# Kernel tuning notes

Hardware: AMD Instinct MI355X
Metric: run time of the kernel (lower is better)

The kernel has to match this reference:

```python
import jax, jax.numpy as jnp
import numpy as np

C_S, C_Z, C_ATOM, H, RBF = 128, 64, 16, 4, 16
N_RES, E_RES, N_ATOM, E_ATOM = 1000, 4000, 14000, 784000


def _p(key, shape, scale=0.05):
    return (jax.random.normal(key, shape, dtype=jnp.float32) * scale)


def setup_inputs() -> dict:
    key = jax.random.key(0)
    ks = jax.random.split(key, 24)
    inp = {
        "node_features": jax.random.normal(ks[0], (N_RES, C_S), dtype=jnp.float32),
        "res_edge_features": jax.random.normal(ks[1], (E_RES, C_Z), dtype=jnp.float32),
        "res_edge_index": jax.random.randint(ks[2], (2, E_RES), 0, N_RES),
        "atom_features": jax.random.normal(ks[3], (N_ATOM, C_ATOM), dtype=jnp.float32),
        "atom_coords": jax.random.normal(ks[4], (N_ATOM, 3), dtype=jnp.float32),
        "cross_atom_edge_index": jax.random.randint(ks[5], (2, E_ATOM), 0, N_ATOM),
        "atom_edge_to_res_edge": jax.random.randint(ks[6], (E_ATOM,), 0, E_RES),
        # atom_dist_embed MLP: RBF -> RBF -> RBF -> H
        "rbf_w1": _p(ks[7], (RBF, RBF)), "rbf_b1": jnp.zeros((RBF,), jnp.float32),
        "rbf_w2": _p(ks[8], (RBF, RBF)), "rbf_b2": jnp.zeros((RBF,), jnp.float32),
        "rbf_w3": _p(ks[9], (RBF, H)),  "rbf_b3": jnp.zeros((H,), jnp.float32),
        # res_level_bias MLP: (2*c_s + c_z) -> c_atom -> H
        "rb_w1": _p(ks[10], (2 * C_S + C_Z, C_ATOM)), "rb_b1": jnp.zeros((C_ATOM,), jnp.float32),
        "rb_w2": _p(ks[11], (C_ATOM, H)), "rb_b2": jnp.zeros((H,), jnp.float32),
        # q / kv / out projections
        "wq": _p(ks[12], (C_ATOM, C_ATOM * H)),     "bq": jnp.zeros((C_ATOM * H,), jnp.float32),
        "wkv": _p(ks[13], (C_ATOM, 2 * C_ATOM * H)), "bkv": jnp.zeros((2 * C_ATOM * H,), jnp.float32),
        "wo": _p(ks[14], (C_ATOM * H, C_ATOM)),     "bo": jnp.zeros((C_ATOM,), jnp.float32),
    }
    return inp


def _rbf(d, d_min=0.0, d_max=20.0, d_count=RBF):
    mu = jnp.linspace(d_min, d_max, d_count, dtype=jnp.float32)
    sigma = (d_max - d_min) / d_count
    return jnp.exp(-(((d[..., None] - mu) / sigma) ** 2))


def _seg_softmax(x, idx, n_seg):
    # scatter-softmax over segments (pyg_utils.softmax), per head column
    m = jax.ops.segment_max(x, idx, num_segments=n_seg)
    e = jnp.exp(x - m[idx])
    s = jax.ops.segment_sum(e, idx, num_segments=n_seg)
    return e / (s[idx] + 1e-16)


def reference(node_features, res_edge_features, res_edge_index, atom_features,
              atom_coords, cross_atom_edge_index, atom_edge_to_res_edge,
              rbf_w1, rbf_b1, rbf_w2, rbf_b2, rbf_w3, rbf_b3,
              rb_w1, rb_b1, rb_w2, rb_b2, wq, bq, wkv, bkv, wo, bo,
              eps=1e-8):
    src = cross_atom_edge_index[1]
    dst = cross_atom_edge_index[0]

    # RBF distance bias  [E_atom, H]
    vec = atom_coords[dst] - atom_coords[src]
    d = jnp.linalg.norm(vec + eps, axis=-1)
    h = jax.nn.relu(_rbf(d) @ rbf_w1 + rbf_b1)
    h = jax.nn.relu(h @ rbf_w2 + rbf_b2)
    atom_dist_bias = h @ rbf_w3 + rbf_b3

    # residue-level bias  [E_res, H]
    cat = jnp.concatenate([res_edge_features,
                           node_features[res_edge_index[0]],
                           node_features[res_edge_index[1]]], axis=-1)
    res_level_bias = jax.nn.relu(cat @ rb_w1 + rb_b1) @ rb_w2 + rb_b2

    # gathered q / k / v  [E_atom, H, c_atom]
    q = (atom_features @ wq + bq)[src].reshape(-1, H, C_ATOM)
    kv = (atom_features @ wkv + bkv)[dst].reshape(-1, H, 2 * C_ATOM)
    k, v = kv[..., :C_ATOM], kv[..., C_ATOM:]

    R = jnp.einsum('ehc,ehc->eh', q, k) / np.sqrt(C_ATOM)
    R = R + res_level_bias[atom_edge_to_res_edge] + atom_dist_bias

    # atom-level scatter-softmax over edges grouped by src atom
    alpha = _seg_softmax(R, src, N_ATOM)

    # residue-level: scatter-mean of scores per residue edge, then softmax by dst res
    cnt = jax.ops.segment_sum(jnp.ones((R.shape[0],), R.dtype),
                              atom_edge_to_res_edge, num_segments=E_RES)
    block_r = jax.ops.segment_sum(R, atom_edge_to_res_edge, num_segments=E_RES)
    block_r = block_r / jnp.clip(cnt, 1.0)[:, None]
    beta = _seg_softmax(block_r, res_edge_index[1], N_RES)

    w = alpha * beta[atom_edge_to_res_edge]           # [E_atom, H]
    atom_update = jax.ops.segment_sum(w[..., None] * v, src, num_segments=N_ATOM)
    return atom_update.reshape(-1, H * C_ATOM) @ wo + bo
```

## Files before the change

### kernel.cpp

```cpp
#include <hip/hip_runtime.h>

#define NH 4
#define N_RES 1000
#define E_RES 4000
#define N_ATOM 14000
#define E_ATOM 784000
#define MAXS 128
#define NBRE 256
#define TABN 16385
#define TINV 512.0f
#define NHB 256
#define EPB 3063

#define PROJ_BLKS ((N_ATOM * 192 + 255) / 256)
#define RLB_BLKS (E_RES / 4)
#define TAB_BLKS ((TABN + 255) / 256)

typedef float f32x4 __attribute__((ext_vector_type(4)));

__device__ __forceinline__ unsigned enc_f(float f) {
  unsigned u = __float_as_uint(f);
  return (u & 0x80000000u) ? ~u : (u | 0x80000000u);
}
__device__ __forceinline__ float dec_f(unsigned e) {
  unsigned u = (e & 0x80000000u) ? (e & 0x7FFFFFFFu) : ~e;
  return __uint_as_float(u);
}

__global__ __launch_bounds__(256) void k_hist(const int* __restrict__ cei,
                                              unsigned* __restrict__ ghistP) {
  __shared__ unsigned lhist[N_ATOM / 2];
  int b = blockIdx.x, t = threadIdx.x;
  for (int j = t; j < N_ATOM / 2; j += 256) lhist[j] = 0u;
  __syncthreads();
  int e0 = b * EPB, e1 = e0 + EPB;
  if (e1 > E_ATOM) e1 = E_ATOM;
  for (int e = e0 + t; e < e1; e += 256) {
    int src = cei[E_ATOM + e];
    atomicAdd(&lhist[src >> 1], (src & 1) ? 65536u : 1u);
  }
  __syncthreads();
  unsigned* gh = ghistP + (size_t)b * (N_ATOM / 2);
  for (int j = t; j < N_ATOM / 2; j += 256) gh[j] = lhist[j];
}

__global__ __launch_bounds__(256) void kA2(
    const float* __restrict__ af, const float* __restrict__ wq,
    const float* __restrict__ bq, const float* __restrict__ wkv,
    const float* __restrict__ bkv, float* __restrict__ Qa,
    float* __restrict__ Ka, float* __restrict__ Va,
    const float* __restrict__ ref_, const float* __restrict__ nf,
    const int* __restrict__ rei, const float* __restrict__ w1,
    const float* __restrict__ b1, const float* __restrict__ w2,
    const float* __restrict__ b2, float* __restrict__ rlb,
    const float* __restrict__ rw1, const float* __restrict__ rb1,
    const float* __restrict__ rw2, const float* __restrict__ rb2,
    const float* __restrict__ rw3, const float* __restrict__ rb3,
    f32x4* __restrict__ tab) {
  __shared__ float hid[4][16];
  int b = blockIdx.x;
  if (b < PROJ_BLKS) {
    int tid = b * 256 + threadIdx.x;
    if (tid < N_ATOM * 192) {
      int a = tid / 192, j = tid % 192;
      const float* row = af + a * 16;
      if (j < 64) {
        float acc = bq[j];
#pragma unroll
        for (int i = 0; i < 16; ++i) acc += row[i] * wq[i * 64 + j];
        Qa[a * 64 + j] = acc;
      } else if (j < 128) {
        int jj = j - 64;
        int col = ((jj >> 4) << 5) + (jj & 15);
        float acc = bkv[col];
#pragma unroll
        for (int i = 0; i < 16; ++i) acc += row[i] * wkv[i * 128 + col];
        Ka[a * 64 + jj] = acc;
      } else {
        int jj = j - 128;
        int col = ((jj >> 4) << 5) + 16 + (jj & 15);
        float acc = bkv[col];
#pragma unroll
        for (int i = 0; i < 16; ++i) acc += row[i] * wkv[i * 128 + col];
        Va[a * 64 + jj] = acc;
      }
    }
  } else if (b < PROJ_BLKS + RLB_BLKS) {
    int sub = threadIdx.x >> 6, l = threadIdx.x & 63;
    int r = (b - PROJ_BLKS) * 4 + sub;
    int r0 = rei[r], r1 = rei[E_RES + r];
    int j = l >> 2, pq = l & 3;
    float acc = 0.f;
    for (int i = pq; i < 320; i += 4) {
      float cc;
      if (i < 64) cc = ref_[r * 64 + i];
      else if (i < 192) cc = nf[r0 * 128 + (i - 64)];
      else cc = nf[r1 * 128 + (i - 192)];
      acc += cc * w1[i * 16 + j];
    }
    acc += __shfl_xor(acc, 1);
    acc += __shfl_xor(acc, 2);
    if (pq == 0) hid[sub][j] = fmaxf(acc + b1[j], 0.f);
    __syncthreads();
    if (l < 4) {
      float o = b2[l];
#pragma unroll
      for (int jj = 0; jj < 16; ++jj) o += hid[sub][jj] * w2[jj * 4 + l];
      rlb[r * 4 + l] = o;
    }
  } else {
    int i = (b - PROJ_BLKS - RLB_BLKS) * 256 + threadIdx.x;
    if (i < TABN) {
      float d = (float)i * (1.0f / TINV);
      float rb[16], h1[16], h2[16];
      const float step = 20.0f / 15.0f;
      const float inv_sigma = 1.0f / 1.25f;
#pragma unroll
      for (int jj = 0; jj < 16; ++jj) {
        float t = (d - jj * step) * inv_sigma;
        rb[jj] = __expf(-t * t);
      }
#pragma unroll
      for (int k = 0; k < 16; ++k) {
        float acc = rb1[k];
#pragma unroll
        for (int jj = 0; jj < 16; ++jj) acc += rb[jj] * rw1[jj * 16 + k];
        h1[k] = fmaxf(acc, 0.f);
      }
#pragma unroll
      for (int k = 0; k < 16; ++k) {
        float acc = rb2[k];
#pragma unroll
        for (int jj = 0; jj < 16; ++jj) acc += h1[jj] * rw2[jj * 16 + k];
        h2[k] = fmaxf(acc, 0.f);
      }
      f32x4 o;
#pragma unroll
      for (int h = 0; h < NH; ++h) {
        float acc = rb3[h];
#pragma unroll
        for (int jj = 0; jj < 16; ++jj) acc += h2[jj] * rw3[jj * 4 + h];
        o[h] = acc;
      }
      tab[i] = o;
    }
  }
}

__global__ __launch_bounds__(256) void k_ofs(const unsigned* __restrict__ ghistP,
                                             unsigned short* __restrict__ ofs16,
                                             int* __restrict__ cnt_src) {
  int s = blockIdx.x * blockDim.x + threadIdx.x;
  if (s >= N_ATOM) return;
  int half = s >> 1;
  unsigned sel = (s & 1) ? 16 : 0;
  int run = 0;
#pragma unroll 8
  for (int b = 0; b < NHB; ++b) {
    int v = (int)((ghistP[(size_t)b * (N_ATOM / 2) + half] >> sel) & 0xFFFFu);
    ofs16[(size_t)b * N_ATOM + s] = (unsigned short)run;
    run += v;
  }
  cnt_src[s] = (run > MAXS) ? MAXS : run;
}

__global__ __launch_bounds__(256) void k_scat(
    const int* __restrict__ cei, const int* __restrict__ aer,
    const unsigned* __restrict__ ofs16P, unsigned* __restrict__ pay) {
  __shared__ int lbase[N_ATOM];
  int b = blockIdx.x, t = threadIdx.x;
  const unsigned* orow = ofs16P + (size_t)b * (N_ATOM / 2);
  for (int j = t; j < N_ATOM / 2; j += 256) {
    unsigned v = orow[j];
    lbase[2 * j] = (int)(v & 0xFFFFu);
    lbase[2 * j + 1] = (int)(v >> 16);
  }
  __syncthreads();
  int e0 = b * EPB, e1 = e0 + EPB;
  if (e1 > E_ATOM) e1 = E_ATOM;
  for (int e = e0 + t; e < e1; e += 256) {
    int src = cei[E_ATOM + e];
    int dst = cei[e];
    int re = aer[e];
    int slot = atomicAdd(&lbase[src], 1);
    if (slot < MAXS)
      pay[(size_t)src * MAXS + slot] = (unsigned)dst | ((unsigned)re << 16);
  }
}

__global__ __launch_bounds__(256) void k_edgeR(
    const int* __restrict__ cnt_src, const unsigned* __restrict__ pay,
    const float* __restrict__ coords, const float* __restrict__ Qa,
    const float* __restrict__ Ka, const float* __restrict__ rlb,
    const f32x4* __restrict__ tab, float* __restrict__ R_slab,
    f32x4* __restrict__ msm, f32x4* __restrict__ mss) {
  int l = threadIdx.x & 63;
  int a = blockIdx.x * 4 + (threadIdx.x >> 6);
  int n = cnt_src[a];
  if (n > MAXS) n = MAXS;
  size_t base = (size_t)a * MAXS;
  float ax = coords[a * 3 + 0], ay = coords[a * 3 + 1], az = coords[a * 3 + 2];
  const float4* qp = (const float4*)(Qa + (size_t)a * 64);
  bool a0 = l < n, a1 = l + 64 < n;
  f32x4 R0, R1;
#pragma unroll
  for (int sl = 0; sl < 2; ++sl) {
    bool act = sl ? a1 : a0;
    f32x4 Rv = {-3.0e38f, -3.0e38f, -3.0e38f, -3.0e38f};
    if (act) {
      int s = l + sl * 64;
      unsigned pr = pay[base + s];
      int dst = (int)(pr & 0xFFFFu);
      int re = (int)(pr >> 16);
      float vx = coords[dst * 3 + 0] - ax + 1e-8f;
      float vy = coords[dst * 3 + 1] - ay + 1e-8f;
      float vz = coords[dst * 3 + 2] - az + 1e-8f;
      float d = sqrtf(vx * vx + vy * vy + vz * vz);
      float x = d * TINV;
      int i = (int)x;
      if (i > TABN - 2) i = TABN - 2;
      float fr = x - (float)i;
      f32x4 t0 = tab[i], t1 = tab[i + 1];
      f32x4 adb = t0 + (t1 - t0) * fr;
      const float4* kp = (const float4*)(Ka + (size_t)dst * 64);
      float4 rlb4 = *(const float4*)(rlb + re * 4);
      const float* rlbp = (const float*)&rlb4;
#pragma unroll
      for (int h = 0; h < NH; ++h) {
        float dot = 0.f;
#pragma unroll
        for (int v4 = 0; v4 < 4; ++v4) {
          float4 q4 = qp[h * 4 + v4];
          float4 k4 = kp[h * 4 + v4];
          dot += q4.x * k4.x + q4.y * k4.y + q4.z * k4.z + q4.w * k4.w;
        }
        Rv[h] = dot * 0.25f + rlbp[h] + adb[h];
      }
      __builtin_nontemporal_store(Rv, (f32x4*)(R_slab + (base + s) * 4));
    }
    if (sl) R1 = Rv; else R0 = Rv;
  }
  f32x4 mx;
#pragma unroll
  for (int h = 0; h < NH; ++h) mx[h] = fmaxf(R0[h], R1[h]);
#pragma unroll
  for (int off = 1; off < 64; off <<= 1) {
#pragma unroll
    for (int h = 0; h < NH; ++h) mx[h] = fmaxf(mx[h], __shfl_xor(mx[h], off));
  }
  f32x4 ex;
#pragma unroll
  for (int h = 0; h < NH; ++h)
    ex[h] = (a0 ? __expf(R0[h] - mx[h]) : 0.f) +
            (a1 ? __expf(R1[h] - mx[h]) : 0.f);
#pragma unroll
  for (int off = 1; off < 64; off <<= 1) {
#pragma unroll
    for (int h = 0; h < NH; ++h) ex[h] += __shfl_xor(ex[h], off);
  }
  if (l == 0) {
    msm[a] = mx;
    mss[a] = ex;
  }
}

__global__ __launch_bounds__(1024) void k_re2(
    const int* __restrict__ cnt_src, const unsigned* __restrict__ pay,
    const float* __restrict__ R_slab, unsigned short* __restrict__ cntg16,
    float* __restrict__ br_g) {
  __shared__ unsigned scntP[E_RES / 2];
  __shared__ float sbr[E_RES * 4];
  int tid = threadIdx.x;
  int bid = blockIdx.x;
  int wv = tid >> 6, lane = tid & 63;
  int gw = bid * 16 + wv;
  for (int j = tid; j < E_RES / 2; j += 1024) scntP[j] = 0u;
  for (int j = tid; j < E_RES * 4; j += 1024) sbr[j] = 0.f;
  __syncthreads();
  for (int a = gw; a < N_ATOM; a += NBRE * 16) {
    int n = cnt_src[a];
    if (n > MAXS) n = MAXS;
    size_t base = (size_t)a * MAXS;
    for (int i = lane; i < n; i += 64) {
      int re = (int)(pay[base + i] >> 16);
      atomicAdd(&scntP[re >> 1], (re & 1) ? 65536u : 1u);
      f32x4 r = *(const f32x4*)(R_slab + (base + i) * 4);
      atomicAdd(&sbr[re * 4 + 0], r[0]);
      atomicAdd(&sbr[re * 4 + 1], r[1]);
      atomicAdd(&sbr[re * 4 + 2], r[2]);
      atomicAdd(&sbr[re * 4 + 3], r[3]);
    }
  }
  __syncthreads();
  for (int j = tid; j < E_RES; j += 1024) {
    unsigned v = scntP[j >> 1];
    cntg16[(size_t)bid * E_RES + j] =
        (unsigned short)((j & 1) ? (v >> 16) : (v & 0xFFFFu));
  }
  for (int j = tid; j < E_RES * 4; j += 1024)
    br_g[(size_t)bid * E_RES * 4 + j] = sbr[j];
}

__global__ __launch_bounds__(256) void k_red(
    const float* __restrict__ br_g, const unsigned short* __restrict__ cntg16,
    float* __restrict__ block_r) {
  int t = blockIdx.x * blockDim.x + threadIdx.x;
  if (t >= E_RES * 4) return;
  int r = t >> 2;
  float s = 0.f;
  int c = 0;
  for (int b = 0; b < NBRE; ++b) {
    s += br_g[(size_t)b * E_RES * 4 + t];
    c += (int)cntg16[(size_t)b * E_RES + r];
  }
  block_r[t] = s / fmaxf((float)c, 1.0f);
}

__global__ __launch_bounds__(1024) void k_br23(
    const float* __restrict__ block_r, const int* __restrict__ rei,
    float* __restrict__ beta) {
  __shared__ unsigned resm[N_RES * 4];
  __shared__ float ress[N_RES * 4];
  int tid = threadIdx.x;
  for (int j = tid; j < N_RES * 4; j += 1024) { resm[j] = 0u; ress[j] = 0.f; }
  __syncthreads();
  float brv[4][4];
  int r1v[4];
  for (int k = 0; k < 4; ++k) {
    int r = tid + k * 1024;
    if (r < E_RES) {
      r1v[k] = rei[E_RES + r];
#pragma unroll
      for (int h = 0; h < 4; ++h) {
        brv[k][h] = block_r[r * 4 + h];
        atomicMax(&resm[r1v[k] * 4 + h], enc_f(brv[k][h]));
      }
    }
  }
  __syncthreads();
  for (int k = 0; k < 4; ++k) {
    int r = tid + k * 1024;
    if (r < E_RES) {
#pragma unroll
      for (int h = 0; h < 4; ++h)
        atomicAdd(&ress[r1v[k] * 4 + h],
                  __expf(brv[k][h] - dec_f(resm[r1v[k] * 4 + h])));
    }
  }
  __syncthreads();
  for (int k = 0; k < 4; ++k) {
    int r = tid + k * 1024;
    if (r < E_RES) {
#pragma unroll
      for (int h = 0; h < 4; ++h)
        beta[r * 4 + h] = __expf(brv[k][h] - dec_f(resm[r1v[k] * 4 + h])) /
                          (ress[r1v[k] * 4 + h] + 1e-16f);
    }
  }
}

__global__ __launch_bounds__(256) void k_src(
    const int* __restrict__ cnt_src, const unsigned* __restrict__ pay,
    const float* __restrict__ R_slab, const float* __restrict__ beta,
    const float* __restrict__ Va, const f32x4* __restrict__ msm,
    const f32x4* __restrict__ mss, const float* __restrict__ wo,
    const float* __restrict__ bo, float* __restrict__ out) {
  __shared__ float sau[4][64];
  int wv = threadIdx.x >> 6, l = threadIdx.x & 63;
  int wid = blockIdx.x * 4 + wv;
  int n = cnt_src[wid];
  if (n > MAXS) n = MAXS;
  int h = l >> 4;
  size_t rbase = (size_t)wid * MAXS;
  f32x4 m4 = msm[wid], s4 = mss[wid];
  float mh = m4[h];
  float sden = s4[h] + 1e-16f;
  float acc = 0.f;
#pragma unroll 4
  for (int i = 0; i < n; ++i) {
    unsigned pr = pay[rbase + i];
    int dst = (int)(pr & 0xFFFFu);
    int re = (int)(pr >> 16);
    float rv = R_slab[(rbase + i) * 4 + h];
    float bt = beta[re * 4 + h];
    float v = Va[(size_t)dst * 64 + l];
    acc += __expf(rv - mh) * bt * v;
  }
  sau[wv][l] = acc / sden;
  __syncthreads();
  int p = l >> 4, c = l & 15;
  float part = 0.f;
#pragma unroll
  for (int jj = 0; jj < 16; ++jj)
    part += sau[wv][p * 16 + jj] * wo[(p * 16 + jj) * 16 + c];
  part += __shfl_down(part, 32);
  part += __shfl_down(part, 16);
  if (l < 16) out[wid * 16 + c] = part + bo[c];
}

extern "C" void kernel_launch(void* const* d_in, const int* in_sizes, int n_in,
                              void* d_out, int out_size, void* d_ws,
                              size_t ws_size, hipStream_t stream) {
  const float* nf   = (const float*)d_in[0];
  const float* ref_ = (const float*)d_in[1];
  const int*   rei  = (const int*)d_in[2];
  const float* af   = (const float*)d_in[3];
  const float* co   = (const float*)d_in[4];
  const int*   cei  = (const int*)d_in[5];
  const int*   aer  = (const int*)d_in[6];
  const float* rw1  = (const float*)d_in[7];
  const float* rb1  = (const float*)d_in[8];
  const float* rw2  = (const float*)d_in[9];
  const float* rb2  = (const float*)d_in[10];
  const float* rw3  = (const float*)d_in[11];
  const float* rb3  = (const float*)d_in[12];
  const float* w1   = (const float*)d_in[13];
  const float* b1   = (const float*)d_in[14];
  const float* w2   = (const float*)d_in[15];
  const float* b2   = (const float*)d_in[16];
  const float* wq   = (const float*)d_in[17];
  const float* bq   = (const float*)d_in[18];
  const float* wkv  = (const float*)d_in[19];
  const float* bkv  = (const float*)d_in[20];
  const float* wo   = (const float*)d_in[21];
  const float* bo   = (const float*)d_in[22];
  float* out = (float*)d_out;

  float* ws = (float*)d_ws;
  float*    Qa      = ws;
  float*    Ka      = Qa + 896000;
  float*    Va      = Ka + 896000;
  float*    rlb     = Va + 896000;
  float*    R_slab  = rlb + 16000;
  unsigned* pay     = (unsigned*)(R_slab + 7168000);
  float*    br_g    = (float*)(pay + 1792000);
  unsigned short* cntg16 = (unsigned short*)(br_g + 4096000);
  int*      cnt_src = (int*)(cntg16 + 1024000);
  float*    block_r = (float*)(cnt_src + 14000);
  f32x4*    tab     = (f32x4*)(block_r + 16000);
  f32x4*    msm     = (f32x4*)((float*)tab + 65544);
  f32x4*    mss     = (f32x4*)((float*)msm + 56000);
  unsigned* ghistP  = (unsigned*)br_g;
  unsigned short* ofs16 = (unsigned short*)R_slab;
  float*    beta    = Ka + 16000;

  k_hist<<<NHB, 256, 0, stream>>>(cei, ghistP);
  kA2<<<PROJ_BLKS + RLB_BLKS + TAB_BLKS, 256, 0, stream>>>(
      af, wq, bq, wkv, bkv, Qa, Ka, Va, ref_, nf, rei, w1, b1, w2, b2, rlb,
      rw1, rb1, rw2, rb2, rw3, rb3, tab);
  k_ofs<<<(N_ATOM + 255) / 256, 256, 0, stream>>>(ghistP, ofs16, cnt_src);
  k_scat<<<NHB, 256, 0, stream>>>(cei, aer, (const unsigned*)ofs16, pay);
  k_edgeR<<<N_ATOM / 4, 256, 0, stream>>>(cnt_src, pay, co, Qa, Ka, rlb, tab,
                                          R_slab, msm, mss);
  k_re2<<<NBRE, 1024, 0, stream>>>(cnt_src, pay, R_slab, cntg16, br_g);
  k_red<<<(E_RES * 4 + 255) / 256, 256, 0, stream>>>(br_g, cntg16, block_r);
  k_br23<<<1, 1024, 0, stream>>>(block_r, rei, beta);
  k_src<<<N_ATOM / 4, 256, 0, stream>>>(cnt_src, pay, R_slab, beta, Va, msm,
                                        mss, wo, bo, out);
}
```

Measured before the change: 237.5 us.

## Split projection kernel, stage weights in LDS, serialize edgeR per-edge with online softmax

Splits the fused projection/bias/table kernel into a projection kernel that caches weights and atom rows in shared memory and a separate bias/table kernel that stages w1 in padded LDS and reads inputs as float4. Pads coordinates to float4 inside the histogram kernel. Rewrites the edge score kernel so each wavefront loops over its edges one at a time, with lanes spread across the 64 head-channels. Dot products use shuffle reductions and the softmax max and sum are computed online. This gives coalesced K-row loads but serializes up to 128 iterations per atom and adds per-edge shuffles, which may cost more than the old edge-parallel layout.

```diff
diff --git a/kernel.cpp b/kernel.cpp
--- a/kernel.cpp
+++ b/kernel.cpp
@@ -12,7 +12,6 @@
 #define NHB 256
 #define EPB 3063
 
-#define PROJ_BLKS ((N_ATOM * 192 + 255) / 256)
 #define RLB_BLKS (E_RES / 4)
 #define TAB_BLKS ((TABN + 255) / 256)
 
@@ -28,7 +27,9 @@
 }
 
 __global__ __launch_bounds__(256) void k_hist(const int* __restrict__ cei,
-                                              unsigned* __restrict__ ghistP) {
+                                              const float* __restrict__ co,
+                                              unsigned* __restrict__ ghistP,
+                                              f32x4* __restrict__ coords4) {
   __shared__ unsigned lhist[N_ATOM / 2];
   int b = blockIdx.x, t = threadIdx.x;
   for (int j = t; j < N_ATOM / 2; j += 256) lhist[j] = 0u;
@@ -39,16 +40,56 @@
     int src = cei[E_ATOM + e];
     atomicAdd(&lhist[src >> 1], (src & 1) ? 65536u : 1u);
   }
+  for (int a = b * 256 + t; a < N_ATOM; a += NHB * 256) {
+    f32x4 c = {co[a * 3 + 0], co[a * 3 + 1], co[a * 3 + 2], 0.f};
+    coords4[a] = c;
+  }
   __syncthreads();
   unsigned* gh = ghistP + (size_t)b * (N_ATOM / 2);
   for (int j = t; j < N_ATOM / 2; j += 256) gh[j] = lhist[j];
 }
 
-__global__ __launch_bounds__(256) void kA2(
+__global__ __launch_bounds__(256) void k_proj(
     const float* __restrict__ af, const float* __restrict__ wq,
     const float* __restrict__ bq, const float* __restrict__ wkv,
     const float* __restrict__ bkv, float* __restrict__ Qa,
-    float* __restrict__ Ka, float* __restrict__ Va,
+    float* __restrict__ Ka, float* __restrict__ Va) {
+  __shared__ float swq[1024], swkv[2048], saf[256];
+  int t = threadIdx.x, b = blockIdx.x;
+  for (int j = t; j < 1024; j += 256) swq[j] = wq[j];
+  for (int j = t; j < 2048; j += 256) swkv[j] = wkv[j];
+  int a0 = b * 16;
+  saf[t] = af[a0 * 16 + t];
+  __syncthreads();
+#pragma unroll
+  for (int k = 0; k < 12; ++k) {
+    int idx = t + k * 256;
+    int al = idx / 192, j = idx % 192;
+    const float* arow = &saf[al * 16];
+    if (j < 64) {
+      float acc = bq[j];
+#pragma unroll
+      for (int i = 0; i < 16; ++i) acc += arow[i] * swq[i * 64 + j];
+      Qa[(size_t)(a0 + al) * 64 + j] = acc;
+    } else if (j < 128) {
+      int jj = j - 64;
+      int col = ((jj >> 4) << 5) + (jj & 15);
+      float acc = bkv[col];
+#pragma unroll
+      for (int i = 0; i < 16; ++i) acc += arow[i] * swkv[i * 128 + col];
+      Ka[(size_t)(a0 + al) * 64 + jj] = acc;
+    } else {
+      int jj = j - 128;
+      int col = ((jj >> 4) << 5) + 16 + (jj & 15);
+      float acc = bkv[col];
+#pragma unroll
+      for (int i = 0; i < 16; ++i) acc += arow[i] * swkv[i * 128 + col];
+      Va[(size_t)(a0 + al) * 64 + jj] = acc;
+    }
+  }
+}
+
+__global__ __launch_bounds__(256) void k_rlbtab(
     const float* __restrict__ ref_, const float* __restrict__ nf,
     const int* __restrict__ rei, const float* __restrict__ w1,
     const float* __restrict__ b1, const float* __restrict__ w2,
@@ -57,59 +98,44 @@
     const float* __restrict__ rw2, const float* __restrict__ rb2,
     const float* __restrict__ rw3, const float* __restrict__ rb3,
     f32x4* __restrict__ tab) {
-  __shared__ float hid[4][16];
   int b = blockIdx.x;
-  if (b < PROJ_BLKS) {
-    int tid = b * 256 + threadIdx.x;
-    if (tid < N_ATOM * 192) {
-      int a = tid / 192, j = tid % 192;
-      const float* row = af + a * 16;
-      if (j < 64) {
-        float acc = bq[j];
-#pragma unroll
-        for (int i = 0; i < 16; ++i) acc += row[i] * wq[i * 64 + j];
-        Qa[a * 64 + j] = acc;
-      } else if (j < 128) {
-        int jj = j - 64;
-        int col = ((jj >> 4) << 5) + (jj & 15);
-        float acc = bkv[col];
-#pragma unroll
-        for (int i = 0; i < 16; ++i) acc += row[i] * wkv[i * 128 + col];
-        Ka[a * 64 + jj] = acc;
-      } else {
-        int jj = j - 128;
-        int col = ((jj >> 4) << 5) + 16 + (jj & 15);
-        float acc = bkv[col];
-#pragma unroll
-        for (int i = 0; i < 16; ++i) acc += row[i] * wkv[i * 128 + col];
-        Va[a * 64 + jj] = acc;
-      }
-    }
-  } else if (b < PROJ_BLKS + RLB_BLKS) {
-    int sub = threadIdx.x >> 6, l = threadIdx.x & 63;
-    int r = (b - PROJ_BLKS) * 4 + sub;
+  if (b < RLB_BLKS) {
+    __shared__ float sw1[320 * 17];
+    __shared__ float sw2[64];
+    __shared__ float hid[4][16];
+    int t = threadIdx.x;
+    for (int i = t; i < 320; i += 256) {
+#pragma unroll
+      for (int j = 0; j < 16; ++j) sw1[i * 17 + j] = w1[i * 16 + j];
+    }
+    if (t < 64) sw2[t] = w2[t];
+    __syncthreads();
+    int sub = t >> 6, l = t & 63;
+    int r = b * 4 + sub;
     int r0 = rei[r], r1 = rei[E_RES + r];
-    int j = l >> 2, pq = l & 3;
+    int j = l & 15, p = l >> 4;
     float acc = 0.f;
-    for (int i = pq; i < 320; i += 4) {
-      float cc;
-      if (i < 64) cc = ref_[r * 64 + i];
-      else if (i < 192) cc = nf[r0 * 128 + (i - 64)];
-      else cc = nf[r1 * 128 + (i - 192)];
-      acc += cc * w1[i * 16 + j];
-    }
-    acc += __shfl_xor(acc, 1);
-    acc += __shfl_xor(acc, 2);
-    if (pq == 0) hid[sub][j] = fmaxf(acc + b1[j], 0.f);
+    for (int c = p; c < 80; c += 4) {
+      int i = c * 4;
+      const float* srcp = (i < 64) ? (ref_ + r * 64 + i)
+                        : (i < 192 ? (nf + r0 * 128 + (i - 64))
+                                   : (nf + r1 * 128 + (i - 192)));
+      float4 v = *(const float4*)srcp;
+      acc += v.x * sw1[(i + 0) * 17 + j] + v.y * sw1[(i + 1) * 17 + j] +
+             v.z * sw1[(i + 2) * 17 + j] + v.w * sw1[(i + 3) * 17 + j];
+    }
+    acc += __shfl_xor(acc, 16);
+    acc += __shfl_xor(acc, 32);
+    if (p == 0) hid[sub][j] = fmaxf(acc + b1[j], 0.f);
     __syncthreads();
     if (l < 4) {
       float o = b2[l];
 #pragma unroll
-      for (int jj = 0; jj < 16; ++jj) o += hid[sub][jj] * w2[jj * 4 + l];
+      for (int jj = 0; jj < 16; ++jj) o += hid[sub][jj] * sw2[jj * 4 + l];
       rlb[r * 4 + l] = o;
     }
   } else {
-    int i = (b - PROJ_BLKS - RLB_BLKS) * 256 + threadIdx.x;
+    int i = (b - RLB_BLKS) * 256 + threadIdx.x;
     if (i < TABN) {
       float d = (float)i * (1.0f / TINV);
       float rb[16], h1[16], h2[16];
@@ -117,8 +143,8 @@
       const float inv_sigma = 1.0f / 1.25f;
 #pragma unroll
       for (int jj = 0; jj < 16; ++jj) {
-        float t = (d - jj * step) * inv_sigma;
-        rb[jj] = __expf(-t * t);
+        float tt = (d - jj * step) * inv_sigma;
+        rb[jj] = __expf(-tt * tt);
       }
 #pragma unroll
       for (int k = 0; k < 16; ++k) {
@@ -190,77 +216,63 @@
 
 __global__ __launch_bounds__(256) void k_edgeR(
     const int* __restrict__ cnt_src, const unsigned* __restrict__ pay,
-    const float* __restrict__ coords, const float* __restrict__ Qa,
+    const f32x4* __restrict__ coords4, const float* __restrict__ Qa,
     const float* __restrict__ Ka, const float* __restrict__ rlb,
     const f32x4* __restrict__ tab, float* __restrict__ R_slab,
     f32x4* __restrict__ msm, f32x4* __restrict__ mss) {
-  int l = threadIdx.x & 63;
-  int a = blockIdx.x * 4 + (threadIdx.x >> 6);
+  int wv = threadIdx.x >> 6, l = threadIdx.x & 63;
+  int a = blockIdx.x * 4 + wv;
   int n = cnt_src[a];
   if (n > MAXS) n = MAXS;
   size_t base = (size_t)a * MAXS;
-  float ax = coords[a * 3 + 0], ay = coords[a * 3 + 1], az = coords[a * 3 + 2];
-  const float4* qp = (const float4*)(Qa + (size_t)a * 64);
-  bool a0 = l < n, a1 = l + 64 < n;
-  f32x4 R0, R1;
-#pragma unroll
-  for (int sl = 0; sl < 2; ++sl) {
-    bool act = sl ? a1 : a0;
-    f32x4 Rv = {-3.0e38f, -3.0e38f, -3.0e38f, -3.0e38f};
-    if (act) {
-      int s = l + sl * 64;
-      unsigned pr = pay[base + s];
-      int dst = (int)(pr & 0xFFFFu);
-      int re = (int)(pr >> 16);
-      float vx = coords[dst * 3 + 0] - ax + 1e-8f;
-      float vy = coords[dst * 3 + 1] - ay + 1e-8f;
-      float vz = coords[dst * 3 + 2] - az + 1e-8f;
-      float d = sqrtf(vx * vx + vy * vy + vz * vz);
-      float x = d * TINV;
-      int i = (int)x;
-      if (i > TABN - 2) i = TABN - 2;
-      float fr = x - (float)i;
-      f32x4 t0 = tab[i], t1 = tab[i + 1];
-      f32x4 adb = t0 + (t1 - t0) * fr;
-      const float4* kp = (const float4*)(Ka + (size_t)dst * 64);
-      float4 rlb4 = *(const float4*)(rlb + re * 4);
-      const float* rlbp = (const float*)&rlb4;
-#pragma unroll
-      for (int h = 0; h < NH; ++h) {
-        float dot = 0.f;
-#pragma unroll
-        for (int v4 = 0; v4 < 4; ++v4) {
-          float4 q4 = qp[h * 4 + v4];
-          float4 k4 = kp[h * 4 + v4];
-          dot += q4.x * k4.x + q4.y * k4.y + q4.z * k4.z + q4.w * k4.w;
-        }
-        Rv[h] = dot * 0.25f + rlbp[h] + adb[h];
-      }
-      __builtin_nontemporal_store(Rv, (f32x4*)(R_slab + (base + s) * 4));
-    }
-    if (sl) R1 = Rv; else R0 = Rv;
-  }
-  f32x4 mx;
-#pragma unroll
-  for (int h = 0; h < NH; ++h) mx[h] = fmaxf(R0[h], R1[h]);
-#pragma unroll
-  for (int off = 1; off < 64; off <<= 1) {
-#pragma unroll
-    for (int h = 0; h < NH; ++h) mx[h] = fmaxf(mx[h], __shfl_xor(mx[h], off));
-  }
-  f32x4 ex;
-#pragma unroll
-  for (int h = 0; h < NH; ++h)
-    ex[h] = (a0 ? __expf(R0[h] - mx[h]) : 0.f) +
-            (a1 ? __expf(R1[h] - mx[h]) : 0.f);
-#pragma unroll
-  for (int off = 1; off < 64; off <<= 1) {
-#pragma unroll
-    for (int h = 0; h < NH; ++h) ex[h] += __shfl_xor(ex[h], off);
-  }
+  float ql = Qa[(size_t)a * 64 + l];
+  f32x4 ac = coords4[a];
+  unsigned prA = (l < n) ? pay[base + l] : 0u;
+  unsigned prB = (l + 64 < n) ? pay[base + 64 + l] : 0u;
+  int h = l >> 4;
+  float m = -3.0e38f, ssum = 0.f;
+#pragma unroll 2
+  for (int s = 0; s < n; ++s) {
+    unsigned pr = __shfl((s < 64) ? prA : prB, s & 63);
+    int dst = (int)(pr & 0xFFFFu);
+    int re = (int)(pr >> 16);
+    float kl = Ka[(size_t)dst * 64 + l];
+    float prod = ql * kl;
+    prod += __shfl_xor(prod, 1);
+    prod += __shfl_xor(prod, 2);
+    prod += __shfl_xor(prod, 4);
+    prod += __shfl_xor(prod, 8);
+    f32x4 c4 = coords4[dst];
+    float vx = c4[0] - ac[0] + 1e-8f;
+    float vy = c4[1] - ac[1] + 1e-8f;
+    float vz = c4[2] - ac[2] + 1e-8f;
+    float d = sqrtf(vx * vx + vy * vy + vz * vz);
+    float x = d * TINV;
+    int i = (int)x;
+    if (i > TABN - 2) i = TABN - 2;
+    float fr = x - (float)i;
+    f32x4 t0 = tab[i], t1 = tab[i + 1];
+    f32x4 adb4 = t0 + (t1 - t0) * fr;
+    float adb = (h < 2) ? ((h == 0) ? adb4[0] : adb4[1])
+                        : ((h == 2) ? adb4[2] : adb4[3]);
+    float rl = rlb[re * 4 + h];
+    float R = prod * 0.25f + rl + adb;
+    float nm = fmaxf(m, R);
+    ssum = ssum * __expf(m - nm) + __expf(R - nm);
+    m = nm;
+    float r1 = __shfl(R, 16), r2 = __shfl(R, 32), r3 = __shfl(R, 48);
+    if (l == 0) {
+      f32x4 v = {R, r1, r2, r3};
+      __builtin_nontemporal_store(v, (f32x4*)(R_slab + (base + s) * 4));
+    }
+  }
+  float m1 = __shfl(m, 16), m2 = __shfl(m, 32), m3 = __shfl(m, 48);
+  float s1 = __shfl(ssum, 16), s2 = __shfl(ssum, 32), s3 = __shfl(ssum, 48);
   if (l == 0) {
-    msm[a] = mx;
-    mss[a] = ex;
+    f32x4 mv = {m, m1, m2, m3};
+    f32x4 sv = {ssum, s1, s2, s3};
+    msm[a] = mv;
+    mss[a] = sv;
   }
 }
 
@@ -440,18 +452,19 @@
   f32x4*    tab     = (f32x4*)(block_r + 16000);
   f32x4*    msm     = (f32x4*)((float*)tab + 65544);
   f32x4*    mss     = (f32x4*)((float*)msm + 56000);
+  f32x4*    coords4 = (f32x4*)((float*)mss + 56000);
   unsigned* ghistP  = (unsigned*)br_g;
   unsigned short* ofs16 = (unsigned short*)R_slab;
   float*    beta    = Ka + 16000;
 
-  k_hist<<<NHB, 256, 0, stream>>>(cei, ghistP);
-  kA2<<<PROJ_BLKS + RLB_BLKS + TAB_BLKS, 256, 0, stream>>>(
-      af, wq, bq, wkv, bkv, Qa, Ka, Va, ref_, nf, rei, w1, b1, w2, b2, rlb,
-      rw1, rb1, rw2, rb2, rw3, rb3, tab);
+  k_hist<<<NHB, 256, 0, stream>>>(cei, co, ghistP, coords4);
+  k_proj<<<N_ATOM / 16, 256, 0, stream>>>(af, wq, bq, wkv, bkv, Qa, Ka, Va);
+  k_rlbtab<<<RLB_BLKS + TAB_BLKS, 256, 0, stream>>>(
+      ref_, nf, rei, w1, b1, w2, b2, rlb, rw1, rb1, rw2, rb2, rw3, rb3, tab);
   k_ofs<<<(N_ATOM + 255) / 256, 256, 0, stream>>>(ghistP, ofs16, cnt_src);
   k_scat<<<NHB, 256, 0, stream>>>(cei, aer, (const unsigned*)ofs16, pay);
-  k_edgeR<<<N_ATOM / 4, 256, 0, stream>>>(cnt_src, pay, co, Qa, Ka, rlb, tab,
-                                          R_slab, msm, mss);
+  k_edgeR<<<N_ATOM / 4, 256, 0, stream>>>(cnt_src, pay, coords4, Qa, Ka, rlb,
+                                          tab, R_slab, msm, mss);
   k_re2<<<NBRE, 1024, 0, stream>>>(cnt_src, pay, R_slab, cntg16, br_g);
   k_red<<<(E_RES * 4 + 255) / 256, 256, 0, stream>>>(br_g, cntg16, block_r);
   k_br23<<<1, 1024, 0, stream>>>(block_r, rei, beta);
```

Result: slower. 368.3 us (+55.1%).
